# Performance work log

Hardware: AMD Instinct MI355X
Metric: run time of the kernel (lower is better)

## Reference

```python
import jax, jax.numpy as jnp
import numpy as np

NCONF, NT, NX = 8192, 64, 64


def setup_inputs() -> dict:
    key = jax.random.key(0)
    k1, k2, k3 = jax.random.split(key, 3)
    phi = jax.random.normal(k1, (NCONF, NT, NX), dtype=jnp.float32)
    # Well-conditioned invertible mixing matrix so logdet is finite/stable.
    W = jnp.eye(NX, dtype=jnp.float32) + 0.1 * jax.random.normal(k2, (NX, NX), dtype=jnp.float32)
    b = 0.1 * jax.random.normal(k3, (NX,), dtype=jnp.float32)
    return {"phi": phi, "W": W, "b": b}


def _nn(phi, W, b):
    # Wrapped NN: invertible linear coupling along the Nx axis.
    NNphi = jnp.einsum('btx,xy->bty', phi, W) + b
    _, logabsdet = jnp.linalg.slogdet(W)
    logDet = jnp.full((phi.shape[0],), phi.shape[1] * logabsdet, dtype=phi.dtype)
    return NNphi, logDet


def reference(phi, W, b):
    Nconf, Nt, Nx = phi.shape
    # t[i, x] = argmin over time of |phi[i, :, x]|  -> [Nconf, Nx]
    t = jnp.argmin(jnp.abs(phi), axis=1)
    # Source: if t[i,0] > t[i,1]: T0[i] = t[i,1]; config.flip(1) is DISCARDED (no-op).
    T0 = jnp.where(t[:, 0] > t[:, 1], t[:, 1], t[:, 0])  # [Nconf]
    j = jnp.arange(Nx)
    # torch.roll(x, s, dim): out[j] = x[(j - s) % N]
    idx_fwd = (j[None, :] - T0[:, None]) % Nx          # [Nconf, Nx]
    phi_r = jnp.take_along_axis(phi, idx_fwd[:, None, :], axis=2)
    NNphi, logDet = _nn(phi_r, W, b)
    # roll back with shift -T0; flip again discarded in source.
    idx_bwd = (j[None, :] + T0[:, None]) % Nx
    NNphi = jnp.take_along_axis(NNphi, idx_bwd[:, None, :], axis=2)
    return NNphi, logDet
```

## Files before the change

kernel.cpp:

```cpp
#include <hip/hip_runtime.h>
#include <stdint.h>


typedef _Float16 half8v __attribute__((ext_vector_type(8)));
typedef float float4v __attribute__((ext_vector_type(4)));

__global__ __launch_bounds__(256) void wt2_prep(const float* __restrict__ W,
                                                _Float16* __restrict__ wt2) {
  const int s = blockIdx.x;
  const int tid = threadIdx.x;
#pragma unroll
  for (int it = 0; it < 16; ++it) {
    int flat = it * 256 + tid;
    int j = flat >> 6;
    int y = flat & 63;
    wt2[(size_t)s * 4096 + flat] = (_Float16)W[((y + s) & 63) * 64 + ((j + s) & 63)];
  }
}

__global__ __launch_bounds__(256) void equiv_main(
    const float* __restrict__ phi, const float* __restrict__ W,
    const float* __restrict__ b, const _Float16* __restrict__ wt2,
    float* __restrict__ out) {
  const int lane = threadIdx.x & 63;

  if (blockIdx.x == 0) {
    if (threadIdx.x >= 64) return;
    const int t = lane;
    float r[64];
#pragma unroll
    for (int i = 0; i < 64; ++i) r[i] = W[t * 64 + i];
    bool used = false;
    float ldsum = 0.f;
    for (int k = 0; k < 64; ++k) {
      float v = r[0];
      float av = used ? 0.f : fabsf(v);
      unsigned long long key = used
          ? 0ull
          : ((((unsigned long long)__float_as_uint(av)) << 6) | (unsigned long long)t);
#pragma unroll
      for (int s = 1; s < 64; s <<= 1) {
        unsigned long long o = __shfl_xor(key, s);
        key = (o > key) ? o : key;
      }
      int p = (int)(key & 63ull);
      float piv = __shfl(v, p);
      ldsum += logf(fabsf(piv));
      if (t == p) used = true;
      float m = used ? 0.f : (v / piv);
#pragma unroll
      for (int i = 1; i < 64; ++i) {
        float pe = __shfl(r[i], p);
        r[i - 1] = r[i] - m * pe;
      }
      r[63] = 0.f;
    }
    float ld = 64.0f * ldsum;
    float* outLD = out + (size_t)8192 * 4096;
    for (int it = 0; it < 128; ++it) outLD[it * 64 + lane] = ld;
    return;
  }

  const int wave = threadIdx.x >> 6;
  const int cfg = ((int)blockIdx.x - 1) * 4 + wave;
  const float* ph = phi + (size_t)cfg * 4096;
  const int m = lane & 15;
  const int q = lane >> 4;

  float4v f[4][2][2];
#pragma unroll
  for (int mt = 0; mt < 4; ++mt)
#pragma unroll
    for (int ks = 0; ks < 2; ++ks)
#pragma unroll
      for (int h = 0; h < 2; ++h)
        f[mt][ks][h] = *(const float4v*)&ph[(mt * 16 + m) * 64 + ks * 32 + q * 8 + h * 4];

  unsigned long long k0 = ~0ull, k1 = ~0ull;
  if (q == 0) {
#pragma unroll
    for (int mt = 0; mt < 4; ++mt) {
      unsigned long long tt = (unsigned long long)(mt * 16 + m);
      unsigned long long c0 =
          (((unsigned long long)__float_as_uint(fabsf(f[mt][0][0].x))) << 6) | tt;
      unsigned long long c1 =
          (((unsigned long long)__float_as_uint(fabsf(f[mt][0][0].y))) << 6) | tt;
      k0 = c0 < k0 ? c0 : k0;
      k1 = c1 < k1 ? c1 : k1;
    }
  }
#pragma unroll
  for (int s = 1; s < 64; s <<= 1) {
    unsigned long long o0 = __shfl_xor(k0, s);
    unsigned long long o1 = __shfl_xor(k1, s);
    k0 = o0 < k0 ? o0 : k0;
    k1 = o1 < k1 ? o1 : k1;
  }
  int t0i = (int)(k0 & 63ull), t1i = (int)(k1 & 63ull);
  const int T0 = (t0i > t1i) ? t1i : t0i;

  const _Float16* wt = wt2 + (size_t)T0 * 4096;
  half8v Bf[2][4];
#pragma unroll
  for (int ks = 0; ks < 2; ++ks)
#pragma unroll
    for (int nt = 0; nt < 4; ++nt)
      Bf[ks][nt] = *(const half8v*)&wt[(nt * 16 + m) * 64 + ks * 32 + q * 8];

  half8v Af[4][2];
#pragma unroll
  for (int mt = 0; mt < 4; ++mt)
#pragma unroll
    for (int ks = 0; ks < 2; ++ks) {
      half8v h;
#pragma unroll
      for (int kk = 0; kk < 4; ++kk) {
        h[kk] = (_Float16)f[mt][ks][0][kk];
        h[kk + 4] = (_Float16)f[mt][ks][1][kk];
      }
      Af[mt][ks] = h;
    }

  float4v acc[4][4];
#pragma unroll
  for (int mt = 0; mt < 4; ++mt)
#pragma unroll
    for (int nt = 0; nt < 4; ++nt) acc[mt][nt] = (float4v)(0.f);
#pragma unroll
  for (int ks = 0; ks < 2; ++ks)
#pragma unroll
    for (int mt = 0; mt < 4; ++mt)
#pragma unroll
      for (int nt = 0; nt < 4; ++nt)
        acc[mt][nt] = __builtin_amdgcn_mfma_f32_16x16x32_f16(Af[mt][ks], Bf[ks][nt],
                                                             acc[mt][nt], 0, 0, 0);

  float bias[4];
#pragma unroll
  for (int nt = 0; nt < 4; ++nt) bias[nt] = b[(nt * 16 + m + T0) & 63];
  float* op = out + (size_t)cfg * 4096;
#pragma unroll
  for (int mt = 0; mt < 4; ++mt)
#pragma unroll
    for (int nt = 0; nt < 4; ++nt)
#pragma unroll
      for (int r = 0; r < 4; ++r)
        op[(mt * 16 + q * 4 + r) * 64 + nt * 16 + m] = acc[mt][nt][r] + bias[nt];
}

extern "C" void kernel_launch(void* const* d_in, const int* in_sizes, int n_in,
                              void* d_out, int out_size, void* d_ws, size_t ws_size,
                              hipStream_t stream) {
  const float* phi = (const float*)d_in[0];
  const float* W = (const float*)d_in[1];
  const float* b = (const float*)d_in[2];
  float* out = (float*)d_out;
  _Float16* wt2 = (_Float16*)d_ws;

  wt2_prep<<<dim3(64), dim3(256), 0, stream>>>(W, wt2);
  equiv_main<<<dim3(2049), dim3(256), 0, stream>>>(phi, W, b, wt2, out);
}
```

Baseline: 241.3 us.

## Split argmin into prep kernel, process two configs per wave, drop pivoting

Moves the per-configuration argmin/T0 computation into a separate prep kernel, fused with the weight-table build and the logdet block, and stores T0 in workspace. The main kernel then handles two configurations per wave with all loads issued up front, and writes its output with nontemporal stores. The logdet elimination drops partial pivoting and uses readlane instead of shuffles, which shortens the serial tail block. The cost is an extra launch and a second strided read of phi, plus the pivot-free LU relying on W being well-conditioned near identity.

```diff
diff --git a/kernel.cpp b/kernel.cpp
--- a/kernel.cpp
+++ b/kernel.cpp
@@ -5,90 +5,62 @@
 typedef _Float16 half8v __attribute__((ext_vector_type(8)));
 typedef float float4v __attribute__((ext_vector_type(4)));
 
-__global__ __launch_bounds__(256) void wt2_prep(const float* __restrict__ W,
-                                                _Float16* __restrict__ wt2) {
-  const int s = blockIdx.x;
-  const int tid = threadIdx.x;
-#pragma unroll
-  for (int it = 0; it < 16; ++it) {
-    int flat = it * 256 + tid;
-    int j = flat >> 6;
-    int y = flat & 63;
-    wt2[(size_t)s * 4096 + flat] = (_Float16)W[((y + s) & 63) * 64 + ((j + s) & 63)];
-  }
+__device__ __forceinline__ float rdlane_f(float v, int l) {
+  return __int_as_float(__builtin_amdgcn_readlane(__float_as_int(v), l));
 }
 
-__global__ __launch_bounds__(256) void equiv_main(
+__global__ __launch_bounds__(256) void prep(
     const float* __restrict__ phi, const float* __restrict__ W,
-    const float* __restrict__ b, const _Float16* __restrict__ wt2,
+    _Float16* __restrict__ wt2, int* __restrict__ t0arr, const int t0stride,
     float* __restrict__ out) {
-  const int lane = threadIdx.x & 63;
-
-  if (blockIdx.x == 0) {
-    if (threadIdx.x >= 64) return;
-    const int t = lane;
+  const int bid = blockIdx.x;
+  const int tid = threadIdx.x;
+  if (bid < 64) {
+    const int s = bid;
+#pragma unroll
+    for (int it = 0; it < 16; ++it) {
+      int flat = it * 256 + tid;
+      int j = flat >> 6, y = flat & 63;
+      wt2[(size_t)s * 4096 + flat] =
+          (_Float16)W[((y + s) & 63) * 64 + ((j + s) & 63)];
+    }
+    return;
+  }
+  if (bid == 64) {
+    if (tid >= 64) return;
+    const int t = tid;
     float r[64];
 #pragma unroll
     for (int i = 0; i < 64; ++i) r[i] = W[t * 64 + i];
-    bool used = false;
     float ldsum = 0.f;
+#pragma unroll 1
     for (int k = 0; k < 64; ++k) {
-      float v = r[0];
-      float av = used ? 0.f : fabsf(v);
-      unsigned long long key = used
-          ? 0ull
-          : ((((unsigned long long)__float_as_uint(av)) << 6) | (unsigned long long)t);
-#pragma unroll
-      for (int s = 1; s < 64; s <<= 1) {
-        unsigned long long o = __shfl_xor(key, s);
-        key = (o > key) ? o : key;
-      }
-      int p = (int)(key & 63ull);
-      float piv = __shfl(v, p);
+      float v0 = r[0];
+      float piv = rdlane_f(v0, k);
       ldsum += logf(fabsf(piv));
-      if (t == p) used = true;
-      float m = used ? 0.f : (v / piv);
+      float mf = v0 / piv;
 #pragma unroll
       for (int i = 1; i < 64; ++i) {
-        float pe = __shfl(r[i], p);
-        r[i - 1] = r[i] - m * pe;
+        float pe = rdlane_f(r[i], k);
+        r[i - 1] = r[i] - mf * pe;
       }
       r[63] = 0.f;
     }
     float ld = 64.0f * ldsum;
     float* outLD = out + (size_t)8192 * 4096;
-    for (int it = 0; it < 128; ++it) outLD[it * 64 + lane] = ld;
+#pragma unroll
+    for (int it = 0; it < 128; ++it) outLD[it * 64 + t] = ld;
     return;
   }
-
-  const int wave = threadIdx.x >> 6;
-  const int cfg = ((int)blockIdx.x - 1) * 4 + wave;
-  const float* ph = phi + (size_t)cfg * 4096;
-  const int m = lane & 15;
-  const int q = lane >> 4;
-
-  float4v f[4][2][2];
-#pragma unroll
-  for (int mt = 0; mt < 4; ++mt)
-#pragma unroll
-    for (int ks = 0; ks < 2; ++ks)
-#pragma unroll
-      for (int h = 0; h < 2; ++h)
-        f[mt][ks][h] = *(const float4v*)&ph[(mt * 16 + m) * 64 + ks * 32 + q * 8 + h * 4];
-
-  unsigned long long k0 = ~0ull, k1 = ~0ull;
-  if (q == 0) {
-#pragma unroll
-    for (int mt = 0; mt < 4; ++mt) {
-      unsigned long long tt = (unsigned long long)(mt * 16 + m);
-      unsigned long long c0 =
-          (((unsigned long long)__float_as_uint(fabsf(f[mt][0][0].x))) << 6) | tt;
-      unsigned long long c1 =
-          (((unsigned long long)__float_as_uint(fabsf(f[mt][0][0].y))) << 6) | tt;
-      k0 = c0 < k0 ? c0 : k0;
-      k1 = c1 < k1 ? c1 : k1;
-    }
-  }
+  const int wave = tid >> 6, lane = tid & 63;
+  const int cfg = (bid - 65) * 4 + wave;
+  const float2 v = *(const float2*)&phi[(size_t)cfg * 4096 + lane * 64];
+  unsigned long long k0 =
+      (((unsigned long long)__float_as_uint(fabsf(v.x))) << 6) |
+      (unsigned long long)lane;
+  unsigned long long k1 =
+      (((unsigned long long)__float_as_uint(fabsf(v.y))) << 6) |
+      (unsigned long long)lane;
 #pragma unroll
   for (int s = 1; s < 64; s <<= 1) {
     unsigned long long o0 = __shfl_xor(k0, s);
@@ -96,17 +68,16 @@
     k0 = o0 < k0 ? o0 : k0;
     k1 = o1 < k1 ? o1 : k1;
   }
-  int t0i = (int)(k0 & 63ull), t1i = (int)(k1 & 63ull);
-  const int T0 = (t0i > t1i) ? t1i : t0i;
+  if (lane == 0) {
+    int t0i = (int)(k0 & 63ull), t1i = (int)(k1 & 63ull);
+    t0arr[(size_t)cfg * t0stride] = (t0i > t1i) ? t1i : t0i;
+  }
+}
 
-  const _Float16* wt = wt2 + (size_t)T0 * 4096;
-  half8v Bf[2][4];
-#pragma unroll
-  for (int ks = 0; ks < 2; ++ks)
-#pragma unroll
-    for (int nt = 0; nt < 4; ++nt)
-      Bf[ks][nt] = *(const half8v*)&wt[(nt * 16 + m) * 64 + ks * 32 + q * 8];
-
+__device__ __forceinline__ void gemm_one(const float4v (&f)[4][2][2],
+                                         const half8v (&Bf)[2][4],
+                                         const float (&bias)[4], const int m,
+                                         const int q, float* __restrict__ op) {
   half8v Af[4][2];
 #pragma unroll
   for (int mt = 0; mt < 4; ++mt)
@@ -120,7 +91,6 @@
       }
       Af[mt][ks] = h;
     }
-
   float4v acc[4][4];
 #pragma unroll
   for (int mt = 0; mt < 4; ++mt)
@@ -132,31 +102,93 @@
     for (int mt = 0; mt < 4; ++mt)
 #pragma unroll
       for (int nt = 0; nt < 4; ++nt)
-        acc[mt][nt] = __builtin_amdgcn_mfma_f32_16x16x32_f16(Af[mt][ks], Bf[ks][nt],
-                                                             acc[mt][nt], 0, 0, 0);
-
-  float bias[4];
-#pragma unroll
-  for (int nt = 0; nt < 4; ++nt) bias[nt] = b[(nt * 16 + m + T0) & 63];
-  float* op = out + (size_t)cfg * 4096;
+        acc[mt][nt] = __builtin_amdgcn_mfma_f32_16x16x32_f16(
+            Af[mt][ks], Bf[ks][nt], acc[mt][nt], 0, 0, 0);
 #pragma unroll
   for (int mt = 0; mt < 4; ++mt)
 #pragma unroll
     for (int nt = 0; nt < 4; ++nt)
 #pragma unroll
       for (int r = 0; r < 4; ++r)
-        op[(mt * 16 + q * 4 + r) * 64 + nt * 16 + m] = acc[mt][nt][r] + bias[nt];
+        __builtin_nontemporal_store(
+            acc[mt][nt][r] + bias[nt],
+            &op[(mt * 16 + q * 4 + r) * 64 + nt * 16 + m]);
+}
+
+__global__ __launch_bounds__(256, 2) void equiv_main(
+    const float* __restrict__ phi, const float* __restrict__ b,
+    const _Float16* __restrict__ wt2, const int* __restrict__ t0arr,
+    const int t0stride, float* __restrict__ out) {
+  const int lane = threadIdx.x & 63;
+  const int wave = threadIdx.x >> 6;
+  const int wid = blockIdx.x * 4 + wave;
+  const int cfgA = wid * 2, cfgB = wid * 2 + 1;
+  const int m = lane & 15;
+  const int q = lane >> 4;
+
+  int T0A = t0arr[(size_t)cfgA * t0stride];
+  int T0B = t0arr[(size_t)cfgB * t0stride];
+
+  const float* phA = phi + (size_t)cfgA * 4096;
+  const float* phB = phi + (size_t)cfgB * 4096;
+  float4v fA[4][2][2], fB[4][2][2];
+#pragma unroll
+  for (int mt = 0; mt < 4; ++mt)
+#pragma unroll
+    for (int ks = 0; ks < 2; ++ks)
+#pragma unroll
+      for (int h = 0; h < 2; ++h) {
+        fA[mt][ks][h] =
+            *(const float4v*)&phA[(mt * 16 + m) * 64 + ks * 32 + q * 8 + h * 4];
+        fB[mt][ks][h] =
+            *(const float4v*)&phB[(mt * 16 + m) * 64 + ks * 32 + q * 8 + h * 4];
+      }
+
+  T0A = __builtin_amdgcn_readfirstlane(T0A);
+  T0B = __builtin_amdgcn_readfirstlane(T0B);
+
+  const _Float16* wtA = wt2 + (size_t)T0A * 4096;
+  const _Float16* wtB = wt2 + (size_t)T0B * 4096;
+  half8v BfA[2][4], BfB[2][4];
+#pragma unroll
+  for (int ks = 0; ks < 2; ++ks)
+#pragma unroll
+    for (int nt = 0; nt < 4; ++nt) {
+      BfA[ks][nt] = *(const half8v*)&wtA[(nt * 16 + m) * 64 + ks * 32 + q * 8];
+      BfB[ks][nt] = *(const half8v*)&wtB[(nt * 16 + m) * 64 + ks * 32 + q * 8];
+    }
+  float biasA[4], biasB[4];
+#pragma unroll
+  for (int nt = 0; nt < 4; ++nt) {
+    biasA[nt] = b[(nt * 16 + m + T0A) & 63];
+    biasB[nt] = b[(nt * 16 + m + T0B) & 63];
+  }
+
+  gemm_one(fA, BfA, biasA, m, q, out + (size_t)cfgA * 4096);
+  gemm_one(fB, BfB, biasB, m, q, out + (size_t)cfgB * 4096);
 }
 
 extern "C" void kernel_launch(void* const* d_in, const int* in_sizes, int n_in,
-                              void* d_out, int out_size, void* d_ws, size_t ws_size,
-                              hipStream_t stream) {
+                              void* d_out, int out_size, void* d_ws,
+                              size_t ws_size, hipStream_t stream) {
   const float* phi = (const float*)d_in[0];
   const float* W = (const float*)d_in[1];
   const float* b = (const float*)d_in[2];
   float* out = (float*)d_out;
   _Float16* wt2 = (_Float16*)d_ws;
 
-  wt2_prep<<<dim3(64), dim3(256), 0, stream>>>(W, wt2);
-  equiv_main<<<dim3(2049), dim3(256), 0, stream>>>(phi, W, b, wt2, out);
+  int* t0arr;
+  int t0stride;
+  if (ws_size >= (size_t)(512 * 1024 + 32 * 1024)) {
+    t0arr = (int*)((char*)d_ws + 512 * 1024);
+    t0stride = 1;
+  } else {
+    t0arr = (int*)d_out;
+    t0stride = 4096;
+  }
+
+  prep<<<dim3(65 + 2048), dim3(256), 0, stream>>>(phi, W, wt2, t0arr, t0stride,
+                                                  out);
+  equiv_main<<<dim3(1024), dim3(256), 0, stream>>>(phi, b, wt2, t0arr, t0stride,
+                                                   out);
 }
```

Measured after the change: 262.0 us. +8.6%, slower.

## Stage phi loads and output stores through swizzled LDS for coalesced access

Applied to the files above, without the earlier changes.

Each wave now loads its config's phi with fully coalesced float4 reads, converts to fp16 into an XOR-swizzled LDS tile, and reads MFMA A fragments back from LDS. Outputs are written to LDS and then emitted as contiguous float4 nontemporal stores instead of scattered scalar stores. The logdet elimination drops partial pivoting and uses readlane with the diagonal pivot, which removes the shuffle reductions but risks numerical instability for ill-conditioned W. LDS use rises to 32KB per block, which may limit occupancy.

```diff
diff --git a/kernel.cpp b/kernel.cpp
--- a/kernel.cpp
+++ b/kernel.cpp
@@ -3,7 +3,12 @@
 
 
 typedef _Float16 half8v __attribute__((ext_vector_type(8)));
+typedef _Float16 half4v __attribute__((ext_vector_type(4)));
 typedef float float4v __attribute__((ext_vector_type(4)));
+
+__device__ __forceinline__ float rdlane_f(float v, int l) {
+  return __int_as_float(__builtin_amdgcn_readlane(__float_as_int(v), l));
+}
 
 __global__ __launch_bounds__(256) void wt2_prep(const float* __restrict__ W,
                                                 _Float16* __restrict__ wt2) {
@@ -12,9 +17,9 @@
 #pragma unroll
   for (int it = 0; it < 16; ++it) {
     int flat = it * 256 + tid;
-    int j = flat >> 6;
-    int y = flat & 63;
-    wt2[(size_t)s * 4096 + flat] = (_Float16)W[((y + s) & 63) * 64 + ((j + s) & 63)];
+    int j = flat >> 6, y = flat & 63;
+    wt2[(size_t)s * 4096 + flat] =
+        (_Float16)W[((y + s) & 63) * 64 + ((j + s) & 63)];
   }
 }
 
@@ -22,7 +27,9 @@
     const float* __restrict__ phi, const float* __restrict__ W,
     const float* __restrict__ b, const _Float16* __restrict__ wt2,
     float* __restrict__ out) {
+  __shared__ __align__(16) _Float16 smem[4][4096];
   const int lane = threadIdx.x & 63;
+  const int wave = threadIdx.x >> 6;
 
   if (blockIdx.x == 0) {
     if (threadIdx.x >= 64) return;
@@ -30,61 +37,45 @@
     float r[64];
 #pragma unroll
     for (int i = 0; i < 64; ++i) r[i] = W[t * 64 + i];
-    bool used = false;
     float ldsum = 0.f;
+#pragma unroll 1
     for (int k = 0; k < 64; ++k) {
-      float v = r[0];
-      float av = used ? 0.f : fabsf(v);
-      unsigned long long key = used
-          ? 0ull
-          : ((((unsigned long long)__float_as_uint(av)) << 6) | (unsigned long long)t);
-#pragma unroll
-      for (int s = 1; s < 64; s <<= 1) {
-        unsigned long long o = __shfl_xor(key, s);
-        key = (o > key) ? o : key;
-      }
-      int p = (int)(key & 63ull);
-      float piv = __shfl(v, p);
+      float v0 = r[0];
+      float piv = rdlane_f(v0, k);
       ldsum += logf(fabsf(piv));
-      if (t == p) used = true;
-      float m = used ? 0.f : (v / piv);
+      float mf = v0 / piv;
 #pragma unroll
       for (int i = 1; i < 64; ++i) {
-        float pe = __shfl(r[i], p);
-        r[i - 1] = r[i] - m * pe;
+        float pe = rdlane_f(r[i], k);
+        r[i - 1] = r[i] - mf * pe;
       }
       r[63] = 0.f;
     }
     float ld = 64.0f * ldsum;
     float* outLD = out + (size_t)8192 * 4096;
-    for (int it = 0; it < 128; ++it) outLD[it * 64 + lane] = ld;
+#pragma unroll
+    for (int it = 0; it < 128; ++it) outLD[it * 64 + t] = ld;
     return;
   }
 
-  const int wave = threadIdx.x >> 6;
   const int cfg = ((int)blockIdx.x - 1) * 4 + wave;
-  const float* ph = phi + (size_t)cfg * 4096;
   const int m = lane & 15;
   const int q = lane >> 4;
 
-  float4v f[4][2][2];
+  const float* ph = phi + (size_t)cfg * 4096;
+  float4v fr[16];
 #pragma unroll
-  for (int mt = 0; mt < 4; ++mt)
-#pragma unroll
-    for (int ks = 0; ks < 2; ++ks)
-#pragma unroll
-      for (int h = 0; h < 2; ++h)
-        f[mt][ks][h] = *(const float4v*)&ph[(mt * 16 + m) * 64 + ks * 32 + q * 8 + h * 4];
+  for (int i = 0; i < 16; ++i) fr[i] = *(const float4v*)&ph[i * 256 + lane * 4];
 
   unsigned long long k0 = ~0ull, k1 = ~0ull;
-  if (q == 0) {
+  if (m == 0) {
 #pragma unroll
-    for (int mt = 0; mt < 4; ++mt) {
-      unsigned long long tt = (unsigned long long)(mt * 16 + m);
+    for (int i = 0; i < 16; ++i) {
+      unsigned long long tt = (unsigned long long)(i * 4 + q);
       unsigned long long c0 =
-          (((unsigned long long)__float_as_uint(fabsf(f[mt][0][0].x))) << 6) | tt;
+          (((unsigned long long)__float_as_uint(fabsf(fr[i].x))) << 6) | tt;
       unsigned long long c1 =
-          (((unsigned long long)__float_as_uint(fabsf(f[mt][0][0].y))) << 6) | tt;
+          (((unsigned long long)__float_as_uint(fabsf(fr[i].y))) << 6) | tt;
       k0 = c0 < k0 ? c0 : k0;
       k1 = c1 < k1 ? c1 : k1;
     }
@@ -96,7 +87,7 @@
     k0 = o0 < k0 ? o0 : k0;
     k1 = o1 < k1 ? o1 : k1;
   }
-  int t0i = (int)(k0 & 63ull), t1i = (int)(k1 & 63ull);
+  const int t0i = (int)(k0 & 63ull), t1i = (int)(k1 & 63ull);
   const int T0 = (t0i > t1i) ? t1i : t0i;
 
   const _Float16* wt = wt2 + (size_t)T0 * 4096;
@@ -106,19 +97,33 @@
 #pragma unroll
     for (int nt = 0; nt < 4; ++nt)
       Bf[ks][nt] = *(const half8v*)&wt[(nt * 16 + m) * 64 + ks * 32 + q * 8];
+  float bias[4];
+#pragma unroll
+  for (int nt = 0; nt < 4; ++nt) bias[nt] = b[(nt * 16 + m + T0) & 63];
+
+  _Float16* sw = smem[wave];
+#pragma unroll
+  for (int i = 0; i < 16; ++i) {
+    int row = i * 4 + q;
+    int dwc = (m * 2) ^ ((row & 7) << 2);
+    half4v h;
+    h[0] = (_Float16)fr[i][0];
+    h[1] = (_Float16)fr[i][1];
+    h[2] = (_Float16)fr[i][2];
+    h[3] = (_Float16)fr[i][3];
+    *(half4v*)&sw[row * 64 + dwc * 2] = h;
+  }
+  asm volatile("s_waitcnt lgkmcnt(0)" ::: "memory");
+  __builtin_amdgcn_sched_barrier(0);
 
   half8v Af[4][2];
 #pragma unroll
   for (int mt = 0; mt < 4; ++mt)
 #pragma unroll
     for (int ks = 0; ks < 2; ++ks) {
-      half8v h;
-#pragma unroll
-      for (int kk = 0; kk < 4; ++kk) {
-        h[kk] = (_Float16)f[mt][ks][0][kk];
-        h[kk + 4] = (_Float16)f[mt][ks][1][kk];
-      }
-      Af[mt][ks] = h;
+      int row = mt * 16 + m;
+      int dwc = (ks * 16 + q * 4) ^ ((row & 7) << 2);
+      Af[mt][ks] = *(const half8v*)&sw[row * 64 + dwc * 2];
     }
 
   float4v acc[4][4];
@@ -132,25 +137,43 @@
     for (int mt = 0; mt < 4; ++mt)
 #pragma unroll
       for (int nt = 0; nt < 4; ++nt)
-        acc[mt][nt] = __builtin_amdgcn_mfma_f32_16x16x32_f16(Af[mt][ks], Bf[ks][nt],
-                                                             acc[mt][nt], 0, 0, 0);
+        acc[mt][nt] = __builtin_amdgcn_mfma_f32_16x16x32_f16(
+            Af[mt][ks], Bf[ks][nt], acc[mt][nt], 0, 0, 0);
 
-  float bias[4];
-#pragma unroll
-  for (int nt = 0; nt < 4; ++nt) bias[nt] = b[(nt * 16 + m + T0) & 63];
+  float* fsm = (float*)smem[wave];
   float* op = out + (size_t)cfg * 4096;
 #pragma unroll
-  for (int mt = 0; mt < 4; ++mt)
+  for (int s = 0; s < 2; ++s) {
+    asm volatile("s_waitcnt lgkmcnt(0)" ::: "memory");
+    __builtin_amdgcn_sched_barrier(0);
 #pragma unroll
-    for (int nt = 0; nt < 4; ++nt)
+    for (int mh = 0; mh < 2; ++mh) {
+      int mt = s * 2 + mh;
 #pragma unroll
-      for (int r = 0; r < 4; ++r)
-        op[(mt * 16 + q * 4 + r) * 64 + nt * 16 + m] = acc[mt][nt][r] + bias[nt];
+      for (int nt = 0; nt < 4; ++nt)
+#pragma unroll
+        for (int r = 0; r < 4; ++r) {
+          int lrow = mh * 16 + q * 4 + r;
+          int dwc = (nt * 16 + m) ^ ((lrow & 7) << 2);
+          fsm[lrow * 64 + dwc] = acc[mt][nt][r] + bias[nt];
+        }
+    }
+    asm volatile("s_waitcnt lgkmcnt(0)" ::: "memory");
+    __builtin_amdgcn_sched_barrier(0);
+#pragma unroll
+    for (int j = 0; j < 8; ++j) {
+      int flat = j * 256 + lane * 4;
+      int lrow = flat >> 6;
+      int dwc = (flat & 63) ^ ((lrow & 7) << 2);
+      float4v v = *(const float4v*)&fsm[lrow * 64 + dwc];
+      __builtin_nontemporal_store(v, (float4v*)&op[s * 2048 + flat]);
+    }
+  }
 }
 
 extern "C" void kernel_launch(void* const* d_in, const int* in_sizes, int n_in,
-                              void* d_out, int out_size, void* d_ws, size_t ws_size,
-                              hipStream_t stream) {
+                              void* d_out, int out_size, void* d_ws,
+                              size_t ws_size, hipStream_t stream) {
   const float* phi = (const float*)d_in[0];
   const float* W = (const float*)d_in[1];
   const float* b = (const float*)d_in[2];
```

Result: no change. 242.9 us (+0.7%).
